# Kernel tuning notes

Hardware: AMD Instinct MI355X
Metric: run time of the kernel (lower is better)

## Reference

```python
import jax, jax.numpy as jnp
import numpy as np
import math

D_MODEL, N_HEADS, D_FF = 1024, 16, 4096
D_K = D_MODEL // N_HEADS
B, S = 4, 2048
EPS = 1e-5


def layer_norm(x, gamma, beta):
    mean = jnp.mean(x, axis=-1, keepdims=True)
    var = jnp.mean((x - mean) ** 2, axis=-1, keepdims=True)  # unbiased=False
    return gamma * (x - mean) / jnp.sqrt(var + EPS) + beta


def setup_inputs() -> dict:
    key = jax.random.key(0)
    ks = jax.random.split(key, 7)
    std_attn = math.sqrt(2.0 / (D_MODEL + D_MODEL))
    std_ff1 = math.sqrt(2.0 / (D_MODEL + D_FF))
    std_ff2 = math.sqrt(2.0 / (D_FF + D_MODEL))
    return {
        "x": jax.random.normal(ks[0], (B, S, D_MODEL), jnp.float32),
        "W_q": jax.random.normal(ks[1], (D_MODEL, D_MODEL), jnp.float32) * std_attn,
        "W_k": jax.random.normal(ks[2], (D_MODEL, D_MODEL), jnp.float32) * std_attn,
        "W_v": jax.random.normal(ks[3], (D_MODEL, D_MODEL), jnp.float32) * std_attn,
        "W_o": jax.random.normal(ks[4], (D_MODEL, D_MODEL), jnp.float32) * std_attn,
        "W1": jax.random.normal(ks[5], (D_MODEL, D_FF), jnp.float32) * std_ff1,
        "b1": jnp.zeros((D_FF,), jnp.float32),
        "W2": jax.random.normal(ks[6], (D_FF, D_MODEL), jnp.float32) * std_ff2,
        "b2": jnp.zeros((D_MODEL,), jnp.float32),
        "ln1_gamma": jnp.ones((D_MODEL,), jnp.float32),
        "ln1_beta": jnp.zeros((D_MODEL,), jnp.float32),
        "ln2_gamma": jnp.ones((D_MODEL,), jnp.float32),
        "ln2_beta": jnp.zeros((D_MODEL,), jnp.float32),
    }


def reference(x, W_q, W_k, W_v, W_o, W1, b1, W2, b2,
              ln1_gamma, ln1_beta, ln2_gamma, ln2_beta):
    b, s, d = x.shape
    # pre-LN attention block
    ln1 = layer_norm(x, ln1_gamma, ln1_beta)
    q = (ln1 @ W_q).reshape(b, s, N_HEADS, D_K)
    k = (ln1 @ W_k).reshape(b, s, N_HEADS, D_K)
    v = (ln1 @ W_v).reshape(b, s, N_HEADS, D_K)
    scores = jnp.einsum("bqhd,bkhd->bhqk", q, k) / math.sqrt(D_K)
    attn = jax.nn.softmax(scores, axis=-1)
    ctx = jnp.einsum("bhqk,bkhd->bqhd", attn, v).reshape(b, s, d)
    attn_out = ctx @ W_o
    attn_residual = x + attn_out
    # pre-LN FFN block
    ln2 = layer_norm(attn_residual, ln2_gamma, ln2_beta)
    ff = jax.nn.relu(ln2 @ W1 + b1) @ W2 + b2
    return attn_residual + ff
```

## Files before the change

kernel.cpp:

```cpp
#include <hip/hip_runtime.h>
#include <hip/hip_bf16.h>

typedef __attribute__((ext_vector_type(4))) float  floatx4;
typedef __attribute__((ext_vector_type(8))) short  shortx8;
typedef __attribute__((ext_vector_type(4))) short  shortx4;

__device__ __forceinline__ short f2bf(float f) {
    unsigned u = __float_as_uint(f);
    u += 0x7fffu + ((u >> 16) & 1u);
    return (short)(u >> 16);
}
__device__ __forceinline__ float bf2f(short s) {
    return __uint_as_float(((unsigned)(unsigned short)s) << 16);
}
__device__ __forceinline__ float fast_exp2(float x) {
#if __has_builtin(__builtin_amdgcn_exp2f)
    return __builtin_amdgcn_exp2f(x);
#else
    return exp2f(x);
#endif
}

__device__ __forceinline__ void load_lds16(const void* g, void* l) {
    __builtin_amdgcn_global_load_lds(
        (const __attribute__((address_space(1))) unsigned int*)g,
        (__attribute__((address_space(3))) unsigned int*)l,
        16, 0, 0);
}

__global__ __launch_bounds__(256)
void transpose_w(const float* __restrict__ src, short* __restrict__ dst, int K, int N)
{
    __shared__ __align__(16) float tile[32][33];
    const int n0 = blockIdx.x * 32, k0 = blockIdx.y * 32;
    const int tx = threadIdx.x & 31, ty = threadIdx.x >> 5;
    for (int i = 0; i < 32; i += 8)
        tile[ty + i][tx] = src[(size_t)(k0 + ty + i) * N + n0 + tx];
    __syncthreads();
    for (int i = 0; i < 32; i += 8)
        dst[(size_t)(n0 + ty + i) * K + k0 + tx] = f2bf(tile[tx][ty + i]);
}

__global__ __launch_bounds__(256)
void ln_bf16(const float* __restrict__ x, const float* __restrict__ g,
             const float* __restrict__ be, short* __restrict__ out)
{
    const int row = blockIdx.x;
    const int tid = threadIdx.x;
    const float4 v = reinterpret_cast<const float4*>(x + (size_t)row * 1024)[tid];
    float s  = v.x + v.y + v.z + v.w;
    float ss = v.x * v.x + v.y * v.y + v.z * v.z + v.w * v.w;
    for (int off = 32; off > 0; off >>= 1) {
        s  += __shfl_down(s,  off);
        ss += __shfl_down(ss, off);
    }
    __shared__ float rs[4], rss[4];
    const int wave = tid >> 6, lane = tid & 63;
    if (lane == 0) { rs[wave] = s; rss[wave] = ss; }
    __syncthreads();
    const float S    = rs[0] + rs[1] + rs[2] + rs[3];
    const float SS   = rss[0] + rss[1] + rss[2] + rss[3];
    const float mean = S * (1.0f / 1024.0f);
    const float var  = SS * (1.0f / 1024.0f) - mean * mean;
    const float rstd = rsqrtf(var + 1e-5f);
    const float4 gg = reinterpret_cast<const float4*>(g)[tid];
    const float4 bb = reinterpret_cast<const float4*>(be)[tid];
    shortx4 o;
    o[0] = f2bf(gg.x * ((v.x - mean) * rstd) + bb.x);
    o[1] = f2bf(gg.y * ((v.y - mean) * rstd) + bb.y);
    o[2] = f2bf(gg.z * ((v.z - mean) * rstd) + bb.z);
    o[3] = f2bf(gg.w * ((v.w - mean) * rstd) + bb.w);
    *reinterpret_cast<shortx4*>(out + (size_t)row * 1024 + tid * 4) = o;
}

template <int EPI>
__global__ __launch_bounds__(256)
void gemm_bt(const short* __restrict__ A, const short* __restrict__ Bt,
             short* __restrict__ Cb, float* __restrict__ Cf,
             const float* __restrict__ bias, const float* __restrict__ resid,
             int M, int N, int K)
{
    __shared__ __align__(16) short As[128 * 32];
    __shared__ __align__(16) short Bs[128 * 32];
    const int tid  = threadIdx.x;
    const int wave = tid >> 6;
    const int lane = tid & 63;
    const int quad = lane >> 4;
    const int l16  = lane & 15;
    const int wm = wave >> 1, wn = wave & 1;
    const size_t bm = (size_t)blockIdx.y * 128;
    const size_t bn = (size_t)blockIdx.x * 128;

    floatx4 acc[4][4];
    for (int i = 0; i < 4; i++)
        for (int j = 0; j < 4; j++)
            acc[i][j] = (floatx4){0.f, 0.f, 0.f, 0.f};

    const int c0 = wave * 2, c1 = wave * 2 + 1;
    const int rA0 = c0 * 16 + (lane >> 2);
    const int rA1 = c1 * 16 + (lane >> 2);
    const int colOff = (lane & 3) * 8;

    for (int k0 = 0; k0 < K; k0 += 32) {
        load_lds16(A  + (bm + rA0) * (size_t)K + k0 + colOff, &As[c0 * 512]);
        load_lds16(A  + (bm + rA1) * (size_t)K + k0 + colOff, &As[c1 * 512]);
        load_lds16(Bt + (bn + rA0) * (size_t)K + k0 + colOff, &Bs[c0 * 512]);
        load_lds16(Bt + (bn + rA1) * (size_t)K + k0 + colOff, &Bs[c1 * 512]);
        __syncthreads();
        shortx8 af[4], bf[4];
        for (int mi = 0; mi < 4; mi++)
            af[mi] = *(const shortx8*)&As[(wm * 64 + mi * 16 + l16) * 32 + quad * 8];
        for (int ni = 0; ni < 4; ni++)
            bf[ni] = *(const shortx8*)&Bs[(wn * 64 + ni * 16 + l16) * 32 + quad * 8];
        for (int mi = 0; mi < 4; mi++)
            for (int ni = 0; ni < 4; ni++)
                acc[mi][ni] = __builtin_amdgcn_mfma_f32_16x16x32_bf16(
                    af[mi], bf[ni], acc[mi][ni], 0, 0, 0);
        __syncthreads();
    }

    for (int mi = 0; mi < 4; mi++) {
        for (int ni = 0; ni < 4; ni++) {
            const size_t row0 = bm + wm * 64 + mi * 16 + quad * 4;
            const size_t col  = bn + wn * 64 + ni * 16 + l16;
            for (int r = 0; r < 4; r++) {
                float v = acc[mi][ni][r];
                const size_t idx = (row0 + r) * (size_t)N + col;
                if (EPI == 0) {
                    Cb[idx] = f2bf(v);
                } else if (EPI == 1) {
                    v += bias[col];
                    Cb[idx] = f2bf(v > 0.f ? v : 0.f);
                } else if (EPI == 2) {
                    Cf[idx] = resid[idx] + v;
                } else {
                    v += bias[col];
                    Cf[idx] = resid[idx] + v;
                }
            }
        }
    }
}

__global__ __launch_bounds__(256)
void transpose_v(const short* __restrict__ qkv, short* __restrict__ vt)
{
    __shared__ __align__(16) short tile[64][65];
    const int st = blockIdx.x, h = blockIdx.y, b = blockIdx.z;
    const int t = threadIdx.x;
    for (int i = 0; i < 2; i++) {
        const int idx = i * 256 + t;
        const int s = idx >> 3, dg = idx & 7;
        shortx8 val = *(const shortx8*)&qkv[(size_t)(b * 2048 + st * 64 + s) * 3072
                                           + 2048 + h * 64 + dg * 8];
        for (int u = 0; u < 8; u++) tile[s][dg * 8 + u] = val[u];
    }
    __syncthreads();
    const int d = t >> 2, sg = (t & 3) * 16;
    shortx8 lo, hi;
    for (int i = 0; i < 8; i++) {
        lo[i] = tile[sg + i][d];
        hi[i] = tile[sg + 8 + i][d];
    }
    const size_t base = ((size_t)(b * 16 + h) * 64 + d) * 2048 + st * 64 + sg;
    *(shortx8*)&vt[base]     = lo;
    *(shortx8*)&vt[base + 8] = hi;
}

__global__ __launch_bounds__(256)
void attention_kernel(const short* __restrict__ qkv, const short* __restrict__ vt,
                      short* __restrict__ ctx)
{
    const int qt = blockIdx.x, h = blockIdx.y, b = blockIdx.z;
    const int tid  = threadIdx.x;
    const int wave = tid >> 6;
    const int lane = tid & 63;
    const int quad = lane >> 4;
    const int l16  = lane & 15;

    __shared__ __align__(16) short Ks[64 * 72];
    __shared__ __align__(16) short Vs[80 * 72];
    __shared__ __align__(16) short Ps[4][32 * 72];

    for (int idx = tid; idx < 16 * 72; idx += 256)
        Vs[64 * 72 + idx] = (short)0x3F80;

    const int q0 = qt * 128 + wave * 32;
    const float qscale = 0.125f * 1.44269504088896f;
    shortx8 qf[2][2];
    for (int qi = 0; qi < 2; qi++) {
        const short* qrow = qkv + (size_t)(b * 2048 + q0 + qi * 16 + l16) * 3072 + h * 64;
        for (int kk = 0; kk < 2; kk++) {
            shortx8 raw = *(const shortx8*)&qrow[kk * 32 + quad * 8];
            for (int j = 0; j < 8; j++) raw[j] = f2bf(bf2f(raw[j]) * qscale);
            qf[qi][kk] = raw;
        }
    }

    floatx4 accO[2][5];
    for (int qi = 0; qi < 2; qi++)
        for (int dt = 0; dt < 5; dt++) accO[qi][dt] = (floatx4){0.f, 0.f, 0.f, 0.f};

    const short* kbase = qkv + (size_t)(b * 2048) * 3072 + 1024 + h * 64;
    const short* vbase = vt + ((size_t)(b * 16 + h) * 64) * 2048;

    for (int kt = 0; kt < 32; ++kt) {
        __syncthreads();
        for (int i = 0; i < 2; i++) {
            const int idx = i * 256 + tid;
            const int s = idx >> 3, dg = idx & 7;
            shortx8 kv = *(const shortx8*)&kbase[(size_t)(kt * 64 + s) * 3072 + dg * 8];
            *(shortx8*)&Ks[s * 72 + dg * 8] = kv;
            shortx8 vv = *(const shortx8*)&vbase[(size_t)s * 2048 + kt * 64 + dg * 8];
            *(shortx8*)&Vs[s * 72 + dg * 8] = vv;
        }
        __syncthreads();

        floatx4 st[4][2];
        for (int nt = 0; nt < 4; nt++) {
            shortx8 kf0 = *(const shortx8*)&Ks[(nt * 16 + l16) * 72 + 0 * 32 + quad * 8];
            shortx8 kf1 = *(const shortx8*)&Ks[(nt * 16 + l16) * 72 + 1 * 32 + quad * 8];
            for (int qi = 0; qi < 2; qi++) {
                floatx4 c = (floatx4){0.f, 0.f, 0.f, 0.f};
                c = __builtin_amdgcn_mfma_f32_16x16x32_bf16(kf0, qf[qi][0], c, 0, 0, 0);
                c = __builtin_amdgcn_mfma_f32_16x16x32_bf16(kf1, qf[qi][1], c, 0, 0, 0);
                st[nt][qi] = c;
            }
        }

        for (int nt = 0; nt < 4; nt++)
            for (int qi = 0; qi < 2; qi++) {
                float2 p01, p23;
                p01.x = fast_exp2(st[nt][qi][0]);
                p01.y = fast_exp2(st[nt][qi][1]);
                p23.x = fast_exp2(st[nt][qi][2]);
                p23.y = fast_exp2(st[nt][qi][3]);
                union { __hip_bfloat162 h2[2]; uint2 u; } pk;
                pk.h2[0] = __float22bfloat162_rn(p01);
                pk.h2[1] = __float22bfloat162_rn(p23);
                *(uint2*)&Ps[wave][(qi * 16 + l16) * 72 + nt * 16 + quad * 4] = pk.u;
            }
        asm volatile("s_waitcnt lgkmcnt(0)" ::: "memory");

        shortx8 pf[2][2];
        for (int qi = 0; qi < 2; qi++)
            for (int kk = 0; kk < 2; kk++)
                pf[qi][kk] = *(const shortx8*)&Ps[wave][(qi * 16 + l16) * 72 + kk * 32 + quad * 8];

        for (int dt = 0; dt < 5; dt++) {
            shortx8 vf0 = *(const shortx8*)&Vs[(dt * 16 + l16) * 72 + 0 * 32 + quad * 8];
            shortx8 vf1 = *(const shortx8*)&Vs[(dt * 16 + l16) * 72 + 1 * 32 + quad * 8];
            for (int qi = 0; qi < 2; qi++) {
                floatx4 c = accO[qi][dt];
                c = __builtin_amdgcn_mfma_f32_16x16x32_bf16(pf[qi][0], vf0, c, 0, 0, 0);
                c = __builtin_amdgcn_mfma_f32_16x16x32_bf16(pf[qi][1], vf1, c, 0, 0, 0);
                accO[qi][dt] = c;
            }
        }
    }

    for (int qi = 0; qi < 2; qi++) {
        const int qg = q0 + qi * 16 + quad * 4;
        for (int r = 0; r < 4; r++) {
            const float inv = 1.0f / accO[qi][4][r];
            for (int dt = 0; dt < 4; dt++)
                ctx[(size_t)(b * 2048 + qg + r) * 1024 + h * 64 + dt * 16 + l16]
                    = f2bf(accO[qi][dt][r] * inv);
        }
    }
}

extern "C" void kernel_launch(void* const* d_in, const int* in_sizes, int n_in,
                              void* d_out, int out_size, void* d_ws, size_t ws_size,
                              hipStream_t stream)
{
    const float* x   = (const float*)d_in[0];
    const float* Wq  = (const float*)d_in[1];
    const float* Wk  = (const float*)d_in[2];
    const float* Wv  = (const float*)d_in[3];
    const float* Wo  = (const float*)d_in[4];
    const float* W1  = (const float*)d_in[5];
    const float* b1  = (const float*)d_in[6];
    const float* W2  = (const float*)d_in[7];
    const float* b2  = (const float*)d_in[8];
    const float* g1  = (const float*)d_in[9];
    const float* be1 = (const float*)d_in[10];
    const float* g2  = (const float*)d_in[11];
    const float* be2 = (const float*)d_in[12];
    float* out = (float*)d_out;
    char*  ws  = (char*)d_ws;

    const size_t MiB = 1u << 20;
    short* regA   = (short*)(ws);
    short* qkv    = (short*)(ws + 16 * MiB);
    short* vt     = (short*)(ws + 64 * MiB);
    short* ff1    = qkv;
    short* Wqkv_t = (short*)(ws + 80 * MiB);
    short* Wo_t   = (short*)(ws + 86 * MiB);
    short* W1_t   = (short*)(ws + 88 * MiB);
    short* W2_t   = (short*)(ws + 96 * MiB);

    const dim3 blk(256);

    transpose_w<<<dim3(32, 32),  blk, 0, stream>>>(Wq, Wqkv_t,                  1024, 1024);
    transpose_w<<<dim3(32, 32),  blk, 0, stream>>>(Wk, Wqkv_t + 1024 * 1024,    1024, 1024);
    transpose_w<<<dim3(32, 32),  blk, 0, stream>>>(Wv, Wqkv_t + 2 * 1024 * 1024,1024, 1024);
    transpose_w<<<dim3(32, 32),  blk, 0, stream>>>(Wo, Wo_t,                    1024, 1024);
    transpose_w<<<dim3(128, 32), blk, 0, stream>>>(W1, W1_t,                    1024, 4096);
    transpose_w<<<dim3(32, 128), blk, 0, stream>>>(W2, W2_t,                    4096, 1024);

    ln_bf16<<<8192, blk, 0, stream>>>(x, g1, be1, regA);
    gemm_bt<0><<<dim3(24, 64), blk, 0, stream>>>(regA, Wqkv_t, qkv, nullptr, nullptr, nullptr,
                                                 8192, 3072, 1024);
    transpose_v<<<dim3(32, 16, 4), blk, 0, stream>>>(qkv, vt);
    attention_kernel<<<dim3(16, 16, 4), blk, 0, stream>>>(qkv, vt, regA);
    gemm_bt<2><<<dim3(8, 64), blk, 0, stream>>>(regA, Wo_t, nullptr, out, nullptr, x,
                                                8192, 1024, 1024);
    ln_bf16<<<8192, blk, 0, stream>>>(out, g2, be2, regA);
    gemm_bt<1><<<dim3(32, 64), blk, 0, stream>>>(regA, W1_t, ff1, nullptr, b1, nullptr,
                                                 8192, 4096, 1024);
    gemm_bt<3><<<dim3(8, 64), blk, 0, stream>>>(ff1, W2_t, nullptr, out, b2, out,
                                                8192, 1024, 4096);
}
```

Measured before the change: 630.3 us.

## Load K/V MFMA fragments directly from global memory, dropping LDS staging and barriers

The attention kernel no longer stages K and V tiles in shared memory behind two block-wide barriers per key tile. Each wave reads its K and V MFMA operands straight from global memory, relying on L1/L2 to serve the reuse across the four waves. The row-sum column of ones is now a register constant instead of padded LDS rows. This removes the sync and LDS round-trip costs but makes each wave issue its own global loads, with more load latency exposed and less explicit reuse.

New measurement: 747.5 us. 18.6% more time.

```diff
diff --git a/kernel.cpp b/kernel.cpp
--- a/kernel.cpp
+++ b/kernel.cpp
@@ -178,12 +178,7 @@
     const int quad = lane >> 4;
     const int l16  = lane & 15;
 
-    __shared__ __align__(16) short Ks[64 * 72];
-    __shared__ __align__(16) short Vs[80 * 72];
     __shared__ __align__(16) short Ps[4][32 * 72];
-
-    for (int idx = tid; idx < 16 * 72; idx += 256)
-        Vs[64 * 72 + idx] = (short)0x3F80;
 
     const int q0 = qt * 128 + wave * 32;
     const float qscale = 0.125f * 1.44269504088896f;
@@ -197,29 +192,23 @@
         }
     }
 
+    shortx8 vones;
+    for (int j = 0; j < 8; j++) vones[j] = (short)0x3F80;
+
     floatx4 accO[2][5];
     for (int qi = 0; qi < 2; qi++)
         for (int dt = 0; dt < 5; dt++) accO[qi][dt] = (floatx4){0.f, 0.f, 0.f, 0.f};
 
     const short* kbase = qkv + (size_t)(b * 2048) * 3072 + 1024 + h * 64;
     const short* vbase = vt + ((size_t)(b * 16 + h) * 64) * 2048;
+    short* const psw = &Ps[wave][0];
 
     for (int kt = 0; kt < 32; ++kt) {
-        __syncthreads();
-        for (int i = 0; i < 2; i++) {
-            const int idx = i * 256 + tid;
-            const int s = idx >> 3, dg = idx & 7;
-            shortx8 kv = *(const shortx8*)&kbase[(size_t)(kt * 64 + s) * 3072 + dg * 8];
-            *(shortx8*)&Ks[s * 72 + dg * 8] = kv;
-            shortx8 vv = *(const shortx8*)&vbase[(size_t)s * 2048 + kt * 64 + dg * 8];
-            *(shortx8*)&Vs[s * 72 + dg * 8] = vv;
-        }
-        __syncthreads();
-
         floatx4 st[4][2];
         for (int nt = 0; nt < 4; nt++) {
-            shortx8 kf0 = *(const shortx8*)&Ks[(nt * 16 + l16) * 72 + 0 * 32 + quad * 8];
-            shortx8 kf1 = *(const shortx8*)&Ks[(nt * 16 + l16) * 72 + 1 * 32 + quad * 8];
+            const short* kp = kbase + (size_t)(kt * 64 + nt * 16 + l16) * 3072 + quad * 8;
+            shortx8 kf0 = *(const shortx8*)kp;
+            shortx8 kf1 = *(const shortx8*)(kp + 32);
             for (int qi = 0; qi < 2; qi++) {
                 floatx4 c = (floatx4){0.f, 0.f, 0.f, 0.f};
                 c = __builtin_amdgcn_mfma_f32_16x16x32_bf16(kf0, qf[qi][0], c, 0, 0, 0);
@@ -238,24 +227,31 @@
                 union { __hip_bfloat162 h2[2]; uint2 u; } pk;
                 pk.h2[0] = __float22bfloat162_rn(p01);
                 pk.h2[1] = __float22bfloat162_rn(p23);
-                *(uint2*)&Ps[wave][(qi * 16 + l16) * 72 + nt * 16 + quad * 4] = pk.u;
+                *(uint2*)&psw[(qi * 16 + l16) * 72 + nt * 16 + quad * 4] = pk.u;
             }
         asm volatile("s_waitcnt lgkmcnt(0)" ::: "memory");
 
         shortx8 pf[2][2];
         for (int qi = 0; qi < 2; qi++)
             for (int kk = 0; kk < 2; kk++)
-                pf[qi][kk] = *(const shortx8*)&Ps[wave][(qi * 16 + l16) * 72 + kk * 32 + quad * 8];
-
-        for (int dt = 0; dt < 5; dt++) {
-            shortx8 vf0 = *(const shortx8*)&Vs[(dt * 16 + l16) * 72 + 0 * 32 + quad * 8];
-            shortx8 vf1 = *(const shortx8*)&Vs[(dt * 16 + l16) * 72 + 1 * 32 + quad * 8];
+                pf[qi][kk] = *(const shortx8*)&psw[(qi * 16 + l16) * 72 + kk * 32 + quad * 8];
+
+        for (int dt = 0; dt < 4; dt++) {
+            const short* vp = vbase + (size_t)(dt * 16 + l16) * 2048 + kt * 64 + quad * 8;
+            shortx8 vf0 = *(const shortx8*)vp;
+            shortx8 vf1 = *(const shortx8*)(vp + 32);
             for (int qi = 0; qi < 2; qi++) {
                 floatx4 c = accO[qi][dt];
                 c = __builtin_amdgcn_mfma_f32_16x16x32_bf16(pf[qi][0], vf0, c, 0, 0, 0);
                 c = __builtin_amdgcn_mfma_f32_16x16x32_bf16(pf[qi][1], vf1, c, 0, 0, 0);
                 accO[qi][dt] = c;
             }
+        }
+        for (int qi = 0; qi < 2; qi++) {
+            floatx4 c = accO[qi][4];
+            c = __builtin_amdgcn_mfma_f32_16x16x32_bf16(pf[qi][0], vones, c, 0, 0, 0);
+            c = __builtin_amdgcn_mfma_f32_16x16x32_bf16(pf[qi][1], vones, c, 0, 0, 0);
+            accO[qi][4] = c;
         }
     }
 
```
